# Performance work log

Measured on AMD Instinct MI355X. Metric: run time of the kernel, lower is better.

## Reference

```python
import jax, jax.numpy as jnp
import numpy as np

PAD_IDX = 0
H = 500  # hidden_size hardcoded in the module
V = 50000
E = 500


def gru_scan(xs, h0, Wih, Whh, bih, bhh):
    """PyTorch-convention GRU over sequence. xs: (S, in), h0: (H,)."""
    def step(h, x):
        gi = x @ Wih.T + bih          # (3H,)
        gh = h @ Whh.T + bhh          # (3H,)
        ir, iz, inn = jnp.split(gi, 3)
        hr, hz, hn = jnp.split(gh, 3)
        r = jax.nn.sigmoid(ir + hr)
        z = jax.nn.sigmoid(iz + hz)
        n = jnp.tanh(inn + r * hn)
        h_new = (1.0 - z) * n + z * h
        return h_new, h_new
    h_last, hs = jax.lax.scan(step, h0, xs)
    return hs, h_last


def setup_inputs() -> dict:
    key = jax.random.key(0)
    ks = jax.random.split(key, 16)
    s = 0.05
    inp = {
        "encoder_input": jax.random.randint(ks[0], (512,), 0, V),
        "target_tensor": jax.random.randint(ks[1], (512,), 0, V),
        "encoder_hidden": jnp.zeros((1, 1, H), jnp.float32),
        # encoder params
        "enc_emb": jax.random.normal(ks[2], (V, E), jnp.float32) * s,
        "enc_Wih": jax.random.normal(ks[3], (3 * H, E), jnp.float32) * s,
        "enc_Whh": jax.random.normal(ks[4], (3 * H, H), jnp.float32) * s,
        "enc_bih": jax.random.normal(ks[5], (3 * H,), jnp.float32) * s,
        "enc_bhh": jax.random.normal(ks[6], (3 * H,), jnp.float32) * s,
        # decoder params
        "dec_emb": jax.random.normal(ks[7], (V, H), jnp.float32) * s,
        "dec_Wih": jax.random.normal(ks[8], (3 * H, H), jnp.float32) * s,
        "dec_Whh": jax.random.normal(ks[9], (3 * H, H), jnp.float32) * s,
        "dec_bih": jax.random.normal(ks[10], (3 * H,), jnp.float32) * s,
        "dec_bhh": jax.random.normal(ks[11], (3 * H,), jnp.float32) * s,
        "out_W": jax.random.normal(ks[12], (V, H), jnp.float32) * s,
        "out_b": jax.random.normal(ks[13], (V,), jnp.float32) * s,
    }
    return inp


def reference(encoder_input, target_tensor, encoder_hidden,
              enc_emb, enc_Wih, enc_Whh, enc_bih, enc_bhh,
              dec_emb, dec_Wih, dec_Whh, dec_bih, dec_bhh,
              out_W, out_b):
    # ---- Encoder: per-token GRU loop == one GRU scan over the sequence ----
    enc_x = enc_emb[encoder_input]                       # (S, E); dropout is identity (p=0 / eval)
    h0 = encoder_hidden[0, 0]                            # (H,)
    _, enc_h = gru_scan(enc_x, h0, enc_Wih, enc_Whh, enc_bih, enc_bhh)

    # ---- Decoder: teacher forcing; input di is target[di-1], first is PAD ----
    dec_in = jnp.concatenate([jnp.array([PAD_IDX], encoder_input.dtype),
                              target_tensor[:-1]])       # (T,)
    dec_x = jax.nn.relu(dec_emb[dec_in])                 # (T, H)
    dec_hs, _ = gru_scan(dec_x, enc_h, dec_Wih, dec_Whh, dec_bih, dec_bhh)  # (T, H)

    logits = dec_hs @ out_W.T + out_b                    # (T, V)
    logp = jax.nn.log_softmax(logits, axis=1)
    T = target_tensor.shape[0]
    # NLLLoss per step (batch=1 -> mean == single value), summed over steps
    loss = -jnp.sum(logp[jnp.arange(T), target_tensor])
    decoder_outputs = jnp.argmax(logp, axis=1).astype(jnp.int64)
    return loss, enc_h.reshape(1, 1, H), decoder_outputs
```

## Files before the change

kernel.cpp:

```cpp
#include <hip/hip_runtime.h>
#include <cstdint>
#include <cstddef>

#define H    500
#define G3   1500
#define SEQ  512
#define V    50000
#define NT   391

#define NB   25
#define HSL  20
#define ROWS 60

static constexpr size_t OFS_HBUF_E = 0;
static constexpr size_t OFS_HBUF_D = 16384;
static constexpr size_t OFS_ENCH   = 32768;
static constexpr size_t OFS_GI_ENC = 65536;
static constexpr size_t OFS_GI_DEC = OFS_GI_ENC + 3276800;
static constexpr size_t OFS_DECHS  = OFS_GI_DEC + 3276800;
static constexpr size_t OFS_SPART  = OFS_DECHS + 1048576;
static constexpr size_t OFS_PPART  = OFS_SPART + 1048576;
static constexpr size_t OFS_LTGT   = OFS_PPART + 2097152;
static constexpr size_t OFS_SFIN   = OFS_LTGT + 4096;

#define GI_BM 64
#define GI_BN 64
#define GI_BK 20
__global__ __launch_bounds__(256) void k_gi_gemm(
    const float* __restrict__ eA, const float* __restrict__ WA,
    const float* __restrict__ bA, const int* __restrict__ tA,
    const float* __restrict__ eB, const float* __restrict__ WB,
    const float* __restrict__ bB, const int* __restrict__ tB,
    float* __restrict__ GiA, float* __restrict__ GiB)
{
    const int dec = blockIdx.z;
    const float* emb = dec ? eB : eA;
    const float* Wih = dec ? WB : WA;
    const float* bih = dec ? bB : bA;
    const int*  toks = dec ? tB : tA;
    float* Gi        = dec ? GiB : GiA;

    __shared__ __align__(16) float As[GI_BK * GI_BM];
    __shared__ __align__(16) float Bs[GI_BK * GI_BN];
    const int tid = threadIdx.x;
    const int n0 = blockIdx.x * GI_BN;
    const int m0 = blockIdx.y * GI_BM;
    const int tx = tid & 15, ty = tid >> 4;
    float acc[4][4] = {};
    for (int k0 = 0; k0 < H; k0 += GI_BK) {
        for (int x = tid; x < 320; x += 256) {
            int m = x / 5, kq = x - m * 5;
            int gm = m0 + m;
            int tok = dec ? ((gm == 0) ? 0 : toks[gm - 1]) : toks[gm];
            float4 v = *(const float4*)(emb + (size_t)tok * H + k0 + kq * 4);
            if (dec) { v.x = fmaxf(v.x, 0.f); v.y = fmaxf(v.y, 0.f);
                       v.z = fmaxf(v.z, 0.f); v.w = fmaxf(v.w, 0.f); }
            int kb = kq * 4;
            As[(kb + 0) * GI_BM + m] = v.x; As[(kb + 1) * GI_BM + m] = v.y;
            As[(kb + 2) * GI_BM + m] = v.z; As[(kb + 3) * GI_BM + m] = v.w;
        }
        for (int x = tid; x < 320; x += 256) {
            int n = x / 5, kq = x - n * 5;
            int gn = n0 + n;
            float4 v = make_float4(0.f, 0.f, 0.f, 0.f);
            if (gn < G3) v = *(const float4*)(Wih + (size_t)gn * H + k0 + kq * 4);
            int kb = kq * 4;
            Bs[(kb + 0) * GI_BN + n] = v.x; Bs[(kb + 1) * GI_BN + n] = v.y;
            Bs[(kb + 2) * GI_BN + n] = v.z; Bs[(kb + 3) * GI_BN + n] = v.w;
        }
        __syncthreads();
#pragma unroll 5
        for (int kk = 0; kk < GI_BK; ++kk) {
            float a[4], b[4];
            *(float4*)&a[0] = *(const float4*)&As[kk * GI_BM + ty * 4];
            *(float4*)&b[0] = *(const float4*)&Bs[kk * GI_BN + tx * 4];
#pragma unroll
            for (int i = 0; i < 4; i++)
#pragma unroll
                for (int j = 0; j < 4; j++) acc[i][j] = fmaf(a[i], b[j], acc[i][j]);
        }
        __syncthreads();
    }
#pragma unroll
    for (int i = 0; i < 4; i++) {
        int gm = m0 + ty * 4 + i;
#pragma unroll
        for (int j = 0; j < 4; j++) {
            int gn = n0 + tx * 4 + j;
            if (gn < G3) Gi[(size_t)gm * G3 + gn] = acc[i][j] + bih[gn];
        }
    }
}

__global__ __launch_bounds__(256, 1) void k_gru(
    const float* __restrict__ Whh, const float* __restrict__ bhh,
    const float* __restrict__ Gi, const float* __restrict__ h0,
    unsigned long long* hbuf, float* hfinal, float* hs_out, float* douth, int S)
{
    __shared__ __align__(16) float h_s[H];
    __shared__ float p_s[ROWS * 26];
    __shared__ float gh_s[ROWS];
    const int tid = threadIdx.x;
    const int wg = blockIdx.x;
    const int j0 = wg * HSL;

    const int g = tid / 25;
    const int s = tid - g * 25;
    const int slc = tid / 10;
    const int e0  = 2 * (tid - slc * 10);

    float wreg[6][20];
    if (tid < 250) {
#pragma unroll
        for (int r = 0; r < 6; ++r) {
            const int rl = g * 6 + r;
            const int gate = rl / 20, jl = rl - gate * 20;
            const float* wr = Whh + (size_t)(gate * 500 + j0 + jl) * H + s * 20;
#pragma unroll
            for (int c = 0; c < 5; ++c)
                *(float4*)&wreg[r][c * 4] = *(const float4*)(wr + c * 4);
        }
    }
    float bb = 0.f;
    if (tid < ROWS) {
        const int gate = tid / 20, jl = tid - gate * 20;
        bb = bhh[gate * 500 + j0 + jl];
    }
    float hown = (tid < HSL) ? h0[j0 + tid] : 0.f;

    if (tid < HSL)
        __hip_atomic_store(hbuf + 800 + wg * 32 + tid,
                           ((unsigned long long)1u << 32) | (unsigned)__float_as_uint(hown),
                           __ATOMIC_RELAXED, __HIP_MEMORY_SCOPE_AGENT);

    for (int t = 0; t < S; ++t) {
        const unsigned want = (unsigned)(t + 1);
        const int rb = (t + 1) & 1;
        float ir = 0.f, iz = 0.f, inn = 0.f;
        if (tid < HSL) {
            const float* gi = Gi + (size_t)t * G3 + j0 + tid;
            ir = gi[0]; iz = gi[500]; inn = gi[1000];
        }
        if (tid < 250) {
            const unsigned long long* pa = hbuf + rb * 800 + slc * 32 + e0;
            unsigned long long v0, v1;
            do {
                v0 = __hip_atomic_load(pa,     __ATOMIC_RELAXED, __HIP_MEMORY_SCOPE_AGENT);
                v1 = __hip_atomic_load(pa + 1, __ATOMIC_RELAXED, __HIP_MEMORY_SCOPE_AGENT);
            } while (((unsigned)(v0 >> 32) != want) || ((unsigned)(v1 >> 32) != want));
            h_s[2 * tid]     = __uint_as_float((unsigned)v0);
            h_s[2 * tid + 1] = __uint_as_float((unsigned)v1);
        }
        __syncthreads();
        if (tid < 250) {
            float hv[20];
#pragma unroll
            for (int c = 0; c < 5; ++c)
                *(float4*)&hv[c * 4] = *(const float4*)&h_s[s * 20 + c * 4];
            float acc[6] = {0.f, 0.f, 0.f, 0.f, 0.f, 0.f};
#pragma unroll
            for (int i = 0; i < 20; ++i)
#pragma unroll
                for (int r = 0; r < 6; ++r) acc[r] = fmaf(wreg[r][i], hv[i], acc[r]);
#pragma unroll
            for (int r = 0; r < 6; ++r) p_s[(g * 6 + r) * 26 + s] = acc[r];
        }
        __syncthreads();
        if (tid < ROWS) {
            float sum = 0.f;
#pragma unroll 5
            for (int i = 0; i < 25; ++i) sum += p_s[tid * 26 + i];
            gh_s[tid] = sum + bb;
        }
        __syncthreads();
        if (tid < HSL) {
            const int j = j0 + tid;
            const float hr = gh_s[tid], hz = gh_s[HSL + tid], hn = gh_s[2 * HSL + tid];
            const float r = 1.f / (1.f + __expf(-(ir + hr)));
            const float z = 1.f / (1.f + __expf(-(iz + hz)));
            const float n = tanhf(inn + r * hn);
            const float hnew = (1.f - z) * n + z * hown;
            hown = hnew;
            __hip_atomic_store(hbuf + (t & 1) * 800 + wg * 32 + tid,
                               ((unsigned long long)(unsigned)(t + 2) << 32) |
                               (unsigned)__float_as_uint(hnew),
                               __ATOMIC_RELAXED, __HIP_MEMORY_SCOPE_AGENT);
            if (hs_out) hs_out[(size_t)t * H + j] = hnew;
            if (t == S - 1) {
                if (hfinal) hfinal[j] = hnew;
                if (douth)  douth[j]  = hnew;
            }
        }
    }
}

#define LG_BM 128
#define LG_BN 128
#define LG_BK 20
__global__ __launch_bounds__(256) void k_logits(
    const float* __restrict__ A, const float* __restrict__ Bw,
    const float* __restrict__ bias,
    float* __restrict__ S_part, unsigned long long* __restrict__ P_part)
{
    __shared__ __align__(16) float As[LG_BK * LG_BM];
    __shared__ __align__(16) float Bs[LG_BK * LG_BN];
    const int tid = threadIdx.x;
    const int bx = blockIdx.x;
    const int n0 = bx * LG_BN;
    const int m0 = blockIdx.y * LG_BM;
    const int tx = tid & 15, ty = tid >> 4;
    float acc[8][8] = {};
    for (int k0 = 0; k0 < H; k0 += LG_BK) {
        for (int x = tid; x < LG_BM * LG_BK; x += 256) {
            int m = x / LG_BK, k = x - m * LG_BK;
            As[k * LG_BM + m] = A[(size_t)(m0 + m) * H + k0 + k];
        }
        for (int x = tid; x < LG_BN * LG_BK; x += 256) {
            int n = x / LG_BK, k = x - n * LG_BK;
            int gn = n0 + n;
            Bs[k * LG_BN + n] = (gn < V) ? Bw[(size_t)gn * H + k0 + k] : 0.f;
        }
        __syncthreads();
#pragma unroll 5
        for (int kk = 0; kk < LG_BK; ++kk) {
            float a[8], b[8];
            *(float4*)&a[0] = *(const float4*)&As[kk * LG_BM + ty * 8];
            *(float4*)&a[4] = *(const float4*)&As[kk * LG_BM + ty * 8 + 4];
            *(float4*)&b[0] = *(const float4*)&Bs[kk * LG_BN + tx * 8];
            *(float4*)&b[4] = *(const float4*)&Bs[kk * LG_BN + tx * 8 + 4];
#pragma unroll
            for (int i = 0; i < 8; i++)
#pragma unroll
                for (int j = 0; j < 8; j++) acc[i][j] = fmaf(a[i], b[j], acc[i][j]);
        }
        __syncthreads();
    }
    float bcol[8]; int gncol[8]; bool bval[8];
#pragma unroll
    for (int j = 0; j < 8; j++) {
        int gn = n0 + tx * 8 + j;
        gncol[j] = gn; bval[j] = gn < V; bcol[j] = bval[j] ? bias[gn] : 0.f;
    }
#pragma unroll
    for (int i = 0; i < 8; i++) {
        int gm = m0 + ty * 8 + i;
        float mx = -3.4e38f; unsigned mi = 0; float se = 0.f;
#pragma unroll
        for (int j = 0; j < 8; j++) {
            if (bval[j]) {
                float l = acc[i][j] + bcol[j];
                se += __expf(l);
                if (l > mx) { mx = l; mi = (unsigned)gncol[j]; }
            }
        }
        unsigned u = __float_as_uint(mx);
        unsigned key = (u & 0x80000000u) ? ~u : (u | 0x80000000u);
        unsigned long long pk = ((unsigned long long)key << 32) |
                                (unsigned long long)(0xFFFFFFFFu - mi);
#pragma unroll
        for (int off = 1; off < 16; off <<= 1) {
            unsigned long long pk2 = __shfl_xor(pk, off);
            se += __shfl_xor(se, off);
            if (pk2 > pk) pk = pk2;
        }
        if (tx == 0) {
            S_part[(size_t)gm * NT + bx] = se;
            P_part[(size_t)gm * NT + bx] = pk;
        }
    }
}

__global__ __launch_bounds__(128) void k_reduce_rows(
    const float* __restrict__ S_part, const unsigned long long* __restrict__ P_part,
    float* __restrict__ Sfin, float* __restrict__ out_argmax)
{
    const int row = blockIdx.x, tid = threadIdx.x;
    float s = 0.f; unsigned long long p = 0ull;
    for (int i = tid; i < NT; i += 128) {
        s += S_part[(size_t)row * NT + i];
        unsigned long long q = P_part[(size_t)row * NT + i];
        if (q > p) p = q;
    }
#pragma unroll
    for (int off = 1; off < 64; off <<= 1) {
        s += __shfl_xor(s, off);
        unsigned long long q = __shfl_xor(p, off);
        if (q > p) p = q;
    }
    __shared__ float s2[2];
    __shared__ unsigned long long p2[2];
    if ((tid & 63) == 0) { s2[tid >> 6] = s; p2[tid >> 6] = p; }
    __syncthreads();
    if (tid == 0) {
        s = s2[0] + s2[1];
        p = p2[0] > p2[1] ? p2[0] : p2[1];
        Sfin[row] = s;
        unsigned idx = 0xFFFFFFFFu - (unsigned)(p & 0xFFFFFFFFull);
        out_argmax[row] = (float)idx;
    }
}

__global__ __launch_bounds__(64) void k_ltgt(
    const float* __restrict__ A, const float* __restrict__ Bw,
    const float* __restrict__ bias, const int* __restrict__ tgt,
    float* __restrict__ ltgt)
{
    const int row = blockIdx.x, lane = threadIdx.x;
    const int tok = tgt[row];
    const float* a = A + (size_t)row * H;
    const float* b = Bw + (size_t)tok * H;
    float s = 0.f;
    for (int k = lane; k < H; k += 64) s = fmaf(a[k], b[k], s);
#pragma unroll
    for (int off = 1; off < 64; off <<= 1) s += __shfl_xor(s, off);
    if (lane == 0) ltgt[row] = s + bias[tok];
}

__global__ __launch_bounds__(512) void k_final(
    const float* __restrict__ Sfin, const float* __restrict__ ltgt, float* __restrict__ d_out)
{
    __shared__ float red[512];
    const int t = threadIdx.x;
    red[t] = logf(Sfin[t]) - ltgt[t];
    __syncthreads();
    for (int s = 256; s > 0; s >>= 1) {
        if (t < s) red[t] += red[t + s];
        __syncthreads();
    }
    if (t == 0) d_out[0] = red[0];
}

extern "C" void kernel_launch(void* const* d_in, const int* in_sizes, int n_in,
                              void* d_out, int out_size, void* d_ws, size_t ws_size,
                              hipStream_t stream) {
    const int*   enc_ids = (const int*)d_in[0];
    const int*   tgt     = (const int*)d_in[1];
    const float* enc_h0  = (const float*)d_in[2];
    const float* enc_emb = (const float*)d_in[3];
    const float* enc_Wih = (const float*)d_in[4];
    const float* enc_Whh = (const float*)d_in[5];
    const float* enc_bih = (const float*)d_in[6];
    const float* enc_bhh = (const float*)d_in[7];
    const float* dec_emb = (const float*)d_in[8];
    const float* dec_Wih = (const float*)d_in[9];
    const float* dec_Whh = (const float*)d_in[10];
    const float* dec_bih = (const float*)d_in[11];
    const float* dec_bhh = (const float*)d_in[12];
    const float* out_W   = (const float*)d_in[13];
    const float* out_b   = (const float*)d_in[14];
    float* out = (float*)d_out;

    char* ws = (char*)d_ws;
    unsigned long long* hbufE = (unsigned long long*)(ws + OFS_HBUF_E);
    unsigned long long* hbufD = (unsigned long long*)(ws + OFS_HBUF_D);
    float* ench   = (float*)(ws + OFS_ENCH);
    float* gi_enc = (float*)(ws + OFS_GI_ENC);
    float* gi_dec = (float*)(ws + OFS_GI_DEC);
    float* dechs  = (float*)(ws + OFS_DECHS);
    float* Spart  = (float*)(ws + OFS_SPART);
    unsigned long long* Ppart = (unsigned long long*)(ws + OFS_PPART);
    float* ltgt   = (float*)(ws + OFS_LTGT);
    float* Sfin   = (float*)(ws + OFS_SFIN);

    k_gi_gemm<<<dim3(24, 8, 2), dim3(256), 0, stream>>>(
        enc_emb, enc_Wih, enc_bih, enc_ids,
        dec_emb, dec_Wih, dec_bih, tgt, gi_enc, gi_dec);
    k_gru<<<dim3(NB), dim3(256), 0, stream>>>(enc_Whh, enc_bhh, gi_enc, enc_h0,
                                              hbufE, ench, (float*)nullptr, out + 1, SEQ);
    k_gru<<<dim3(NB), dim3(256), 0, stream>>>(dec_Whh, dec_bhh, gi_dec, ench,
                                              hbufD, (float*)nullptr, dechs, (float*)nullptr, SEQ);
    k_ltgt<<<dim3(SEQ), dim3(64), 0, stream>>>(dechs, out_W, out_b, tgt, ltgt);
    k_logits<<<dim3(NT, 4), dim3(256), 0, stream>>>(dechs, out_W, out_b, Spart, Ppart);
    k_reduce_rows<<<dim3(SEQ), dim3(128), 0, stream>>>(Spart, Ppart, Sfin, out + 1 + H);
    k_final<<<dim3(1), dim3(512), 0, stream>>>(Sfin, ltgt, out);
}
```

Before: 2.563 ms.

## Fuse encoder/decoder GRU with overlapped decoder-Gi and logits GEMM via work tickets

Merges the encoder and decoder GRU recurrences into one persistent kernel that runs all 1024 steps on 25 blocks. The remaining 231 blocks pull work tickets to compute the decoder input projection and, once each 128-step epoch of decoder hidden states is published, the logits and target-logit tiles for those rows. The aim is to hide the decoder Gi GEMM and the large vocabulary GEMM behind the serial recurrence and to remove launch gaps. This adds spin-wait counters, a separate init kernel, and risks the recurrence blocks being slowed by sharing CUs or memory bandwidth with the GEMM blocks.

```diff
diff --git a/kernel.cpp b/kernel.cpp
--- a/kernel.cpp
+++ b/kernel.cpp
@@ -11,10 +11,14 @@
 #define NB   25
 #define HSL  20
 #define ROWS 60
-
-static constexpr size_t OFS_HBUF_E = 0;
-static constexpr size_t OFS_HBUF_D = 16384;
-static constexpr size_t OFS_ENCH   = 32768;
+#define NBLK 256
+
+#define NGI  192
+#define TPB  (NT + 1)
+#define NTICK (NGI + 4 * TPB)
+
+static constexpr size_t OFS_HBUF   = 0;
+static constexpr size_t OFS_CTRL   = 32768;
 static constexpr size_t OFS_GI_ENC = 65536;
 static constexpr size_t OFS_GI_DEC = OFS_GI_ENC + 3276800;
 static constexpr size_t OFS_DECHS  = OFS_GI_DEC + 3276800;
@@ -23,23 +27,21 @@
 static constexpr size_t OFS_LTGT   = OFS_PPART + 2097152;
 static constexpr size_t OFS_SFIN   = OFS_LTGT + 4096;
 
+__global__ __launch_bounds__(256) void k_init(unsigned long long* hbuf, int* ctrl)
+{
+    const int tid = threadIdx.x;
+    for (int i = tid; i < 1600; i += 256) hbuf[i] = 0ull;
+    if (tid < 8) ctrl[tid] = 0;
+}
+
 #define GI_BM 64
 #define GI_BN 64
 #define GI_BK 20
-__global__ __launch_bounds__(256) void k_gi_gemm(
-    const float* __restrict__ eA, const float* __restrict__ WA,
-    const float* __restrict__ bA, const int* __restrict__ tA,
-    const float* __restrict__ eB, const float* __restrict__ WB,
-    const float* __restrict__ bB, const int* __restrict__ tB,
-    float* __restrict__ GiA, float* __restrict__ GiB)
+__global__ __launch_bounds__(256) void k_gi_enc(
+    const float* __restrict__ emb, const float* __restrict__ Wih,
+    const float* __restrict__ bih, const int* __restrict__ toks,
+    float* __restrict__ Gi)
 {
-    const int dec = blockIdx.z;
-    const float* emb = dec ? eB : eA;
-    const float* Wih = dec ? WB : WA;
-    const float* bih = dec ? bB : bA;
-    const int*  toks = dec ? tB : tA;
-    float* Gi        = dec ? GiB : GiA;
-
     __shared__ __align__(16) float As[GI_BK * GI_BM];
     __shared__ __align__(16) float Bs[GI_BK * GI_BN];
     const int tid = threadIdx.x;
@@ -50,11 +52,8 @@
     for (int k0 = 0; k0 < H; k0 += GI_BK) {
         for (int x = tid; x < 320; x += 256) {
             int m = x / 5, kq = x - m * 5;
-            int gm = m0 + m;
-            int tok = dec ? ((gm == 0) ? 0 : toks[gm - 1]) : toks[gm];
+            int tok = toks[m0 + m];
             float4 v = *(const float4*)(emb + (size_t)tok * H + k0 + kq * 4);
-            if (dec) { v.x = fmaxf(v.x, 0.f); v.y = fmaxf(v.y, 0.f);
-                       v.z = fmaxf(v.z, 0.f); v.w = fmaxf(v.w, 0.f); }
             int kb = kq * 4;
             As[(kb + 0) * GI_BM + m] = v.x; As[(kb + 1) * GI_BM + m] = v.y;
             As[(kb + 2) * GI_BM + m] = v.z; As[(kb + 3) * GI_BM + m] = v.w;
@@ -92,180 +91,319 @@
     }
 }
 
-__global__ __launch_bounds__(256, 1) void k_gru(
-    const float* __restrict__ Whh, const float* __restrict__ bhh,
-    const float* __restrict__ Gi, const float* __restrict__ h0,
-    unsigned long long* hbuf, float* hfinal, float* hs_out, float* douth, int S)
-{
-    __shared__ __align__(16) float h_s[H];
-    __shared__ float p_s[ROWS * 26];
-    __shared__ float gh_s[ROWS];
-    const int tid = threadIdx.x;
-    const int wg = blockIdx.x;
-    const int j0 = wg * HSL;
-
-    const int g = tid / 25;
-    const int s = tid - g * 25;
-    const int slc = tid / 10;
-    const int e0  = 2 * (tid - slc * 10);
-
-    float wreg[6][20];
-    if (tid < 250) {
-#pragma unroll
-        for (int r = 0; r < 6; ++r) {
-            const int rl = g * 6 + r;
-            const int gate = rl / 20, jl = rl - gate * 20;
-            const float* wr = Whh + (size_t)(gate * 500 + j0 + jl) * H + s * 20;
-#pragma unroll
-            for (int c = 0; c < 5; ++c)
-                *(float4*)&wreg[r][c * 4] = *(const float4*)(wr + c * 4);
-        }
-    }
-    float bb = 0.f;
-    if (tid < ROWS) {
-        const int gate = tid / 20, jl = tid - gate * 20;
-        bb = bhh[gate * 500 + j0 + jl];
-    }
-    float hown = (tid < HSL) ? h0[j0 + tid] : 0.f;
-
-    if (tid < HSL)
-        __hip_atomic_store(hbuf + 800 + wg * 32 + tid,
-                           ((unsigned long long)1u << 32) | (unsigned)__float_as_uint(hown),
-                           __ATOMIC_RELAXED, __HIP_MEMORY_SCOPE_AGENT);
-
-    for (int t = 0; t < S; ++t) {
-        const unsigned want = (unsigned)(t + 1);
-        const int rb = (t + 1) & 1;
-        float ir = 0.f, iz = 0.f, inn = 0.f;
-        if (tid < HSL) {
-            const float* gi = Gi + (size_t)t * G3 + j0 + tid;
-            ir = gi[0]; iz = gi[500]; inn = gi[1000];
-        }
-        if (tid < 250) {
-            const unsigned long long* pa = hbuf + rb * 800 + slc * 32 + e0;
-            unsigned long long v0, v1;
-            do {
-                v0 = __hip_atomic_load(pa,     __ATOMIC_RELAXED, __HIP_MEMORY_SCOPE_AGENT);
-                v1 = __hip_atomic_load(pa + 1, __ATOMIC_RELAXED, __HIP_MEMORY_SCOPE_AGENT);
-            } while (((unsigned)(v0 >> 32) != want) || ((unsigned)(v1 >> 32) != want));
-            h_s[2 * tid]     = __uint_as_float((unsigned)v0);
-            h_s[2 * tid + 1] = __uint_as_float((unsigned)v1);
-        }
-        __syncthreads();
-        if (tid < 250) {
-            float hv[20];
-#pragma unroll
-            for (int c = 0; c < 5; ++c)
-                *(float4*)&hv[c * 4] = *(const float4*)&h_s[s * 20 + c * 4];
-            float acc[6] = {0.f, 0.f, 0.f, 0.f, 0.f, 0.f};
-#pragma unroll
-            for (int i = 0; i < 20; ++i)
-#pragma unroll
-                for (int r = 0; r < 6; ++r) acc[r] = fmaf(wreg[r][i], hv[i], acc[r]);
-#pragma unroll
-            for (int r = 0; r < 6; ++r) p_s[(g * 6 + r) * 26 + s] = acc[r];
-        }
-        __syncthreads();
-        if (tid < ROWS) {
-            float sum = 0.f;
-#pragma unroll 5
-            for (int i = 0; i < 25; ++i) sum += p_s[tid * 26 + i];
-            gh_s[tid] = sum + bb;
-        }
-        __syncthreads();
-        if (tid < HSL) {
-            const int j = j0 + tid;
-            const float hr = gh_s[tid], hz = gh_s[HSL + tid], hn = gh_s[2 * HSL + tid];
-            const float r = 1.f / (1.f + __expf(-(ir + hr)));
-            const float z = 1.f / (1.f + __expf(-(iz + hz)));
-            const float n = tanhf(inn + r * hn);
-            const float hnew = (1.f - z) * n + z * hown;
-            hown = hnew;
-            __hip_atomic_store(hbuf + (t & 1) * 800 + wg * 32 + tid,
-                               ((unsigned long long)(unsigned)(t + 2) << 32) |
-                               (unsigned)__float_as_uint(hnew),
-                               __ATOMIC_RELAXED, __HIP_MEMORY_SCOPE_AGENT);
-            if (hs_out) hs_out[(size_t)t * H + j] = hnew;
-            if (t == S - 1) {
-                if (hfinal) hfinal[j] = hnew;
-                if (douth)  douth[j]  = hnew;
-            }
-        }
-    }
-}
-
 #define LG_BM 128
 #define LG_BN 128
 #define LG_BK 20
-__global__ __launch_bounds__(256) void k_logits(
-    const float* __restrict__ A, const float* __restrict__ Bw,
-    const float* __restrict__ bias,
+__global__ __launch_bounds__(256, 1) void k_fused(
+    const float* __restrict__ eWhh, const float* __restrict__ ebhh,
+    const float* __restrict__ GiE,
+    const float* __restrict__ dWhh, const float* __restrict__ dbhh,
+    float* __restrict__ GiD,
+    const float* __restrict__ demb, const float* __restrict__ dWih,
+    const float* __restrict__ dbih, const int* __restrict__ tgt,
+    const float* __restrict__ h0, unsigned long long* hbuf, int* ctrl,
+    float* __restrict__ ench_out, float* __restrict__ dechs,
+    const float* __restrict__ outW, const float* __restrict__ outb,
+    float* __restrict__ ltgt,
     float* __restrict__ S_part, unsigned long long* __restrict__ P_part)
 {
     __shared__ __align__(16) float As[LG_BK * LG_BM];
     __shared__ __align__(16) float Bs[LG_BK * LG_BN];
+    __shared__ __align__(16) float h_s[H];
+    __shared__ float p_s[ROWS * 26];
+    __shared__ float gh_s[ROWS];
+    __shared__ int go_s;
     const int tid = threadIdx.x;
-    const int bx = blockIdx.x;
-    const int n0 = bx * LG_BN;
-    const int m0 = blockIdx.y * LG_BM;
-    const int tx = tid & 15, ty = tid >> 4;
-    float acc[8][8] = {};
-    for (int k0 = 0; k0 < H; k0 += LG_BK) {
-        for (int x = tid; x < LG_BM * LG_BK; x += 256) {
-            int m = x / LG_BK, k = x - m * LG_BK;
-            As[k * LG_BM + m] = A[(size_t)(m0 + m) * H + k0 + k];
-        }
-        for (int x = tid; x < LG_BN * LG_BK; x += 256) {
-            int n = x / LG_BK, k = x - n * LG_BK;
-            int gn = n0 + n;
-            Bs[k * LG_BN + n] = (gn < V) ? Bw[(size_t)gn * H + k0 + k] : 0.f;
-        }
+    int* ticket  = ctrl + 0;
+    int* gi_done = ctrl + 1;
+    int* epoch   = ctrl + 2;
+
+    if (blockIdx.x < NB) {
+        __builtin_amdgcn_s_setprio(2);
+        const int wg = blockIdx.x;
+        const int j0 = wg * HSL;
+        const int g = tid / 25;
+        const int s = tid - g * 25;
+        const int slc = tid / 10;
+        const int e0  = 2 * (tid - slc * 10);
+
+        float wreg[6][20];
+        if (tid < 250) {
+#pragma unroll
+            for (int r = 0; r < 6; ++r) {
+                const int rl = g * 6 + r;
+                const int gate = rl / 20, jl = rl - gate * 20;
+                const float* wr = eWhh + (size_t)(gate * 500 + j0 + jl) * H + s * 20;
+#pragma unroll
+                for (int c = 0; c < 5; ++c)
+                    *(float4*)&wreg[r][c * 4] = *(const float4*)(wr + c * 4);
+            }
+        }
+        float bb = 0.f;
+        if (tid < ROWS) {
+            const int gate = tid / 20, jl = tid - gate * 20;
+            bb = ebhh[gate * 500 + j0 + jl];
+        }
+        float hown = (tid < HSL) ? h0[j0 + tid] : 0.f;
+
+        if (tid < HSL)
+            __hip_atomic_store(hbuf + 800 + wg * 32 + tid,
+                               ((unsigned long long)1u << 32) | (unsigned)__float_as_uint(hown),
+                               __ATOMIC_RELAXED, __HIP_MEMORY_SCOPE_AGENT);
+
+        for (int t = 0; t < 2 * SEQ; ++t) {
+            if (t == SEQ) {
+                if (tid == 0) {
+                    while (__hip_atomic_load(gi_done, __ATOMIC_ACQUIRE,
+                                             __HIP_MEMORY_SCOPE_AGENT) < NGI)
+                        __builtin_amdgcn_s_sleep(8);
+                }
+                __syncthreads();
+                if (tid < 250) {
+#pragma unroll
+                    for (int r = 0; r < 6; ++r) {
+                        const int rl = g * 6 + r;
+                        const int gate = rl / 20, jl = rl - gate * 20;
+                        const float* wr = dWhh + (size_t)(gate * 500 + j0 + jl) * H + s * 20;
+#pragma unroll
+                        for (int c = 0; c < 5; ++c)
+                            *(float4*)&wreg[r][c * 4] = *(const float4*)(wr + c * 4);
+                    }
+                }
+                if (tid < ROWS) {
+                    const int gate = tid / 20, jl = tid - gate * 20;
+                    bb = dbhh[gate * 500 + j0 + jl];
+                }
+            }
+            const unsigned want = (unsigned)(t + 1);
+            const int rb = (t + 1) & 1;
+            float ir = 0.f, iz = 0.f, inn = 0.f;
+            if (tid < HSL) {
+                const float* gi = (t < SEQ ? GiE + (size_t)t * G3
+                                           : GiD + (size_t)(t - SEQ) * G3) + j0 + tid;
+                ir = gi[0]; iz = gi[500]; inn = gi[1000];
+            }
+            if (tid < 250) {
+                const unsigned long long* pa = hbuf + rb * 800 + slc * 32 + e0;
+                unsigned long long v0, v1;
+                do {
+                    v0 = __hip_atomic_load(pa,     __ATOMIC_RELAXED, __HIP_MEMORY_SCOPE_AGENT);
+                    v1 = __hip_atomic_load(pa + 1, __ATOMIC_RELAXED, __HIP_MEMORY_SCOPE_AGENT);
+                } while (((unsigned)(v0 >> 32) != want) || ((unsigned)(v1 >> 32) != want));
+                h_s[2 * tid]     = __uint_as_float((unsigned)v0);
+                h_s[2 * tid + 1] = __uint_as_float((unsigned)v1);
+            }
+            __syncthreads();
+            if (tid < 250) {
+                float hv[20];
+#pragma unroll
+                for (int c = 0; c < 5; ++c)
+                    *(float4*)&hv[c * 4] = *(const float4*)&h_s[s * 20 + c * 4];
+                float acc[6] = {0.f, 0.f, 0.f, 0.f, 0.f, 0.f};
+#pragma unroll
+                for (int i = 0; i < 20; ++i)
+#pragma unroll
+                    for (int r = 0; r < 6; ++r) acc[r] = fmaf(wreg[r][i], hv[i], acc[r]);
+#pragma unroll
+                for (int r = 0; r < 6; ++r) p_s[(g * 6 + r) * 26 + s] = acc[r];
+            }
+            __syncthreads();
+            if (tid < ROWS) {
+                float sum = 0.f;
+#pragma unroll 5
+                for (int i = 0; i < 25; ++i) sum += p_s[tid * 26 + i];
+                gh_s[tid] = sum + bb;
+            }
+            __syncthreads();
+            if (tid < HSL) {
+                const int j = j0 + tid;
+                const float hr = gh_s[tid], hz = gh_s[HSL + tid], hn = gh_s[2 * HSL + tid];
+                const float r = 1.f / (1.f + __expf(-(ir + hr)));
+                const float z = 1.f / (1.f + __expf(-(iz + hz)));
+                const float n = tanhf(inn + r * hn);
+                const float hnew = (1.f - z) * n + z * hown;
+                hown = hnew;
+                __hip_atomic_store(hbuf + (t & 1) * 800 + wg * 32 + tid,
+                                   ((unsigned long long)(unsigned)(t + 2) << 32) |
+                                   (unsigned)__float_as_uint(hnew),
+                                   __ATOMIC_RELAXED, __HIP_MEMORY_SCOPE_AGENT);
+                if (t == SEQ - 1) ench_out[j] = hnew;
+                if (t >= SEQ)
+                    __hip_atomic_store(&dechs[(size_t)(t - SEQ) * H + j], hnew,
+                                       __ATOMIC_RELAXED, __HIP_MEMORY_SCOPE_AGENT);
+            }
+            if (t >= SEQ && ((t - SEQ) & 127) == 127) {
+                __syncthreads();
+                if (tid == 0)
+                    __hip_atomic_fetch_add(&epoch[(t - SEQ) >> 7], 1,
+                                           __ATOMIC_RELEASE, __HIP_MEMORY_SCOPE_AGENT);
+            }
+        }
+        return;
+    }
+
+    int epoch_seen = -1;
+    for (;;) {
         __syncthreads();
+        if (tid == 0) go_s = atomicAdd(ticket, 1);
+        __syncthreads();
+        const int tk = go_s;
+        if (tk >= NTICK) return;
+
+        if (tk < NGI) {
+            const int n0 = (tk % 24) * GI_BN;
+            const int m0 = (tk / 24) * GI_BM;
+            const int tx = tid & 15, ty = tid >> 4;
+            float acc[4][4] = {};
+            for (int k0 = 0; k0 < H; k0 += GI_BK) {
+                for (int x = tid; x < 320; x += 256) {
+                    int m = x / 5, kq = x - m * 5;
+                    int gm = m0 + m;
+                    int tok = (gm == 0) ? 0 : tgt[gm - 1];
+                    float4 v = *(const float4*)(demb + (size_t)tok * H + k0 + kq * 4);
+                    v.x = fmaxf(v.x, 0.f); v.y = fmaxf(v.y, 0.f);
+                    v.z = fmaxf(v.z, 0.f); v.w = fmaxf(v.w, 0.f);
+                    int kb = kq * 4;
+                    As[(kb + 0) * GI_BM + m] = v.x; As[(kb + 1) * GI_BM + m] = v.y;
+                    As[(kb + 2) * GI_BM + m] = v.z; As[(kb + 3) * GI_BM + m] = v.w;
+                }
+                for (int x = tid; x < 320; x += 256) {
+                    int n = x / 5, kq = x - n * 5;
+                    int gn = n0 + n;
+                    float4 v = make_float4(0.f, 0.f, 0.f, 0.f);
+                    if (gn < G3) v = *(const float4*)(dWih + (size_t)gn * H + k0 + kq * 4);
+                    int kb = kq * 4;
+                    Bs[(kb + 0) * GI_BM + n] = v.x; Bs[(kb + 1) * GI_BM + n] = v.y;
+                    Bs[(kb + 2) * GI_BM + n] = v.z; Bs[(kb + 3) * GI_BM + n] = v.w;
+                }
+                __syncthreads();
 #pragma unroll 5
-        for (int kk = 0; kk < LG_BK; ++kk) {
-            float a[8], b[8];
-            *(float4*)&a[0] = *(const float4*)&As[kk * LG_BM + ty * 8];
-            *(float4*)&a[4] = *(const float4*)&As[kk * LG_BM + ty * 8 + 4];
-            *(float4*)&b[0] = *(const float4*)&Bs[kk * LG_BN + tx * 8];
-            *(float4*)&b[4] = *(const float4*)&Bs[kk * LG_BN + tx * 8 + 4];
-#pragma unroll
-            for (int i = 0; i < 8; i++)
-#pragma unroll
-                for (int j = 0; j < 8; j++) acc[i][j] = fmaf(a[i], b[j], acc[i][j]);
-        }
-        __syncthreads();
-    }
-    float bcol[8]; int gncol[8]; bool bval[8];
-#pragma unroll
-    for (int j = 0; j < 8; j++) {
-        int gn = n0 + tx * 8 + j;
-        gncol[j] = gn; bval[j] = gn < V; bcol[j] = bval[j] ? bias[gn] : 0.f;
-    }
-#pragma unroll
-    for (int i = 0; i < 8; i++) {
-        int gm = m0 + ty * 8 + i;
-        float mx = -3.4e38f; unsigned mi = 0; float se = 0.f;
+                for (int kk = 0; kk < GI_BK; ++kk) {
+                    float a[4], b[4];
+                    *(float4*)&a[0] = *(const float4*)&As[kk * GI_BM + ty * 4];
+                    *(float4*)&b[0] = *(const float4*)&Bs[kk * GI_BM + tx * 4];
+#pragma unroll
+                    for (int i = 0; i < 4; i++)
+#pragma unroll
+                        for (int j = 0; j < 4; j++) acc[i][j] = fmaf(a[i], b[j], acc[i][j]);
+                }
+                __syncthreads();
+            }
+#pragma unroll
+            for (int i = 0; i < 4; i++) {
+                int gm = m0 + ty * 4 + i;
+#pragma unroll
+                for (int j = 0; j < 4; j++) {
+                    int gn = n0 + tx * 4 + j;
+                    if (gn < G3)
+                        __hip_atomic_store(&GiD[(size_t)gm * G3 + gn], acc[i][j] + dbih[gn],
+                                           __ATOMIC_RELAXED, __HIP_MEMORY_SCOPE_AGENT);
+                }
+            }
+            __syncthreads();
+            if (tid == 0)
+                __hip_atomic_fetch_add(gi_done, 1, __ATOMIC_RELEASE, __HIP_MEMORY_SCOPE_AGENT);
+            continue;
+        }
+
+        const int tk2 = tk - NGI;
+        const int e = tk2 / TPB;
+        const int r = tk2 - e * TPB;
+        if (e > epoch_seen) {
+            if (tid == 0) {
+                while (__hip_atomic_load(&epoch[e], __ATOMIC_ACQUIRE,
+                                         __HIP_MEMORY_SCOPE_AGENT) < NB)
+                    __builtin_amdgcn_s_sleep(64);
+            }
+            __syncthreads();
+            epoch_seen = e;
+        }
+        const int m0 = e * LG_BM;
+
+        if (r == 0) {
+            const int w = tid >> 6, lane = tid & 63;
+            for (int rr = w; rr < LG_BM; rr += 4) {
+                const int row = m0 + rr;
+                const int tok = tgt[row];
+                const float* a = dechs + (size_t)row * H;
+                const float* b = outW + (size_t)tok * H;
+                float sv = 0.f;
+                for (int k = lane; k < H; k += 64) sv = fmaf(a[k], b[k], sv);
+#pragma unroll
+                for (int off = 1; off < 64; off <<= 1) sv += __shfl_xor(sv, off);
+                if (lane == 0) ltgt[row] = sv + outb[tok];
+            }
+            continue;
+        }
+
+        const int bx = r - 1;
+        const int n0 = bx * LG_BN;
+        const int tx = tid & 15, ty = tid >> 4;
+        float acc[8][8] = {};
+        for (int k0 = 0; k0 < H; k0 += LG_BK) {
+            for (int x = tid; x < 640; x += 256) {
+                int m = x / 5, kq = x - m * 5;
+                float4 v = *(const float4*)(dechs + (size_t)(m0 + m) * H + k0 + kq * 4);
+                int kb = kq * 4;
+                As[(kb + 0) * LG_BM + m] = v.x; As[(kb + 1) * LG_BM + m] = v.y;
+                As[(kb + 2) * LG_BM + m] = v.z; As[(kb + 3) * LG_BM + m] = v.w;
+            }
+            for (int x = tid; x < 640; x += 256) {
+                int n = x / 5, kq = x - n * 5;
+                int gn = n0 + n;
+                float4 v = make_float4(0.f, 0.f, 0.f, 0.f);
+                if (gn < V) v = *(const float4*)(outW + (size_t)gn * H + k0 + kq * 4);
+                int kb = kq * 4;
+                Bs[(kb + 0) * LG_BN + n] = v.x; Bs[(kb + 1) * LG_BN + n] = v.y;
+                Bs[(kb + 2) * LG_BN + n] = v.z; Bs[(kb + 3) * LG_BN + n] = v.w;
+            }
+            __syncthreads();
+#pragma unroll 5
+            for (int kk = 0; kk < LG_BK; ++kk) {
+                float a[8], b[8];
+                *(float4*)&a[0] = *(const float4*)&As[kk * LG_BM + ty * 8];
+                *(float4*)&a[4] = *(const float4*)&As[kk * LG_BM + ty * 8 + 4];
+                *(float4*)&b[0] = *(const float4*)&Bs[kk * LG_BN + tx * 8];
+                *(float4*)&b[4] = *(const float4*)&Bs[kk * LG_BN + tx * 8 + 4];
+#pragma unroll
+                for (int i = 0; i < 8; i++)
+#pragma unroll
+                    for (int j = 0; j < 8; j++) acc[i][j] = fmaf(a[i], b[j], acc[i][j]);
+            }
+            __syncthreads();
+        }
+        float bcol[8]; int gncol[8]; bool bval[8];
 #pragma unroll
         for (int j = 0; j < 8; j++) {
-            if (bval[j]) {
-                float l = acc[i][j] + bcol[j];
-                se += __expf(l);
-                if (l > mx) { mx = l; mi = (unsigned)gncol[j]; }
-            }
-        }
-        unsigned u = __float_as_uint(mx);
-        unsigned key = (u & 0x80000000u) ? ~u : (u | 0x80000000u);
-        unsigned long long pk = ((unsigned long long)key << 32) |
-                                (unsigned long long)(0xFFFFFFFFu - mi);
-#pragma unroll
-        for (int off = 1; off < 16; off <<= 1) {
-            unsigned long long pk2 = __shfl_xor(pk, off);
-            se += __shfl_xor(se, off);
-            if (pk2 > pk) pk = pk2;
-        }
-        if (tx == 0) {
-            S_part[(size_t)gm * NT + bx] = se;
-            P_part[(size_t)gm * NT + bx] = pk;
+            int gn = n0 + tx * 8 + j;
+            gncol[j] = gn; bval[j] = gn < V; bcol[j] = bval[j] ? outb[gn] : 0.f;
+        }
+#pragma unroll
+        for (int i = 0; i < 8; i++) {
+            int gm = m0 + ty * 8 + i;
+            float mx = -3.4e38f; unsigned mi = 0; float se = 0.f;
+#pragma unroll
+            for (int j = 0; j < 8; j++) {
+                if (bval[j]) {
+                    float l = acc[i][j] + bcol[j];
+                    se += __expf(l);
+                    if (l > mx) { mx = l; mi = (unsigned)gncol[j]; }
+                }
+            }
+            unsigned u = __float_as_uint(mx);
+            unsigned key = (u & 0x80000000u) ? ~u : (u | 0x80000000u);
+            unsigned long long pk = ((unsigned long long)key << 32) |
+                                    (unsigned long long)(0xFFFFFFFFu - mi);
+#pragma unroll
+            for (int off = 1; off < 16; off <<= 1) {
+                unsigned long long pk2 = __shfl_xor(pk, off);
+                se += __shfl_xor(se, off);
+                if (pk2 > pk) pk = pk2;
+            }
+            if (tx == 0) {
+                S_part[(size_t)gm * NT + bx] = se;
+                P_part[(size_t)gm * NT + bx] = pk;
+            }
         }
     }
 }
@@ -298,22 +436,6 @@
         unsigned idx = 0xFFFFFFFFu - (unsigned)(p & 0xFFFFFFFFull);
         out_argmax[row] = (float)idx;
     }
-}
-
-__global__ __launch_bounds__(64) void k_ltgt(
-    const float* __restrict__ A, const float* __restrict__ Bw,
-    const float* __restrict__ bias, const int* __restrict__ tgt,
-    float* __restrict__ ltgt)
-{
-    const int row = blockIdx.x, lane = threadIdx.x;
-    const int tok = tgt[row];
-    const float* a = A + (size_t)row * H;
-    const float* b = Bw + (size_t)tok * H;
-    float s = 0.f;
-    for (int k = lane; k < H; k += 64) s = fmaf(a[k], b[k], s);
-#pragma unroll
-    for (int off = 1; off < 64; off <<= 1) s += __shfl_xor(s, off);
-    if (lane == 0) ltgt[row] = s + bias[tok];
 }
 
 __global__ __launch_bounds__(512) void k_final(
@@ -351,9 +473,8 @@
     float* out = (float*)d_out;
 
     char* ws = (char*)d_ws;
-    unsigned long long* hbufE = (unsigned long long*)(ws + OFS_HBUF_E);
-    unsigned long long* hbufD = (unsigned long long*)(ws + OFS_HBUF_D);
-    float* ench   = (float*)(ws + OFS_ENCH);
+    unsigned long long* hbuf = (unsigned long long*)(ws + OFS_HBUF);
+    int*   ctrl   = (int*)(ws + OFS_CTRL);
     float* gi_enc = (float*)(ws + OFS_GI_ENC);
     float* gi_dec = (float*)(ws + OFS_GI_DEC);
     float* dechs  = (float*)(ws + OFS_DECHS);
@@ -362,15 +483,15 @@
     float* ltgt   = (float*)(ws + OFS_LTGT);
     float* Sfin   = (float*)(ws + OFS_SFIN);
 
-    k_gi_gemm<<<dim3(24, 8, 2), dim3(256), 0, stream>>>(
-        enc_emb, enc_Wih, enc_bih, enc_ids,
-        dec_emb, dec_Wih, dec_bih, tgt, gi_enc, gi_dec);
-    k_gru<<<dim3(NB), dim3(256), 0, stream>>>(enc_Whh, enc_bhh, gi_enc, enc_h0,
-                                              hbufE, ench, (float*)nullptr, out + 1, SEQ);
-    k_gru<<<dim3(NB), dim3(256), 0, stream>>>(dec_Whh, dec_bhh, gi_dec, ench,
-                                              hbufD, (float*)nullptr, dechs, (float*)nullptr, SEQ);
-    k_ltgt<<<dim3(SEQ), dim3(64), 0, stream>>>(dechs, out_W, out_b, tgt, ltgt);
-    k_logits<<<dim3(NT, 4), dim3(256), 0, stream>>>(dechs, out_W, out_b, Spart, Ppart);
+    k_init<<<dim3(1), dim3(256), 0, stream>>>(hbuf, ctrl);
+    k_gi_enc<<<dim3(24, 8), dim3(256), 0, stream>>>(enc_emb, enc_Wih, enc_bih,
+                                                    enc_ids, gi_enc);
+    k_fused<<<dim3(NBLK), dim3(256), 0, stream>>>(
+        enc_Whh, enc_bhh, gi_enc,
+        dec_Whh, dec_bhh, gi_dec,
+        dec_emb, dec_Wih, dec_bih, tgt,
+        enc_h0, hbuf, ctrl, out + 1, dechs,
+        out_W, out_b, ltgt, Spart, Ppart);
     k_reduce_rows<<<dim3(SEQ), dim3(128), 0, stream>>>(Spart, Ppart, Sfin, out + 1 + H);
     k_final<<<dim3(1), dim3(512), 0, stream>>>(Sfin, ltgt, out);
 }
```

After: 3.323 ms. +29.7%, slower.
